# Kernel optimization log

Hardware: AMD Instinct MI355X
Metric: run time of the kernel (lower is better)

The kernel has to match this reference:

```python
import jax, jax.numpy as jnp
import numpy as np

ALPHA = 0.05        # per-layer ternary scale folded into the compact weight
FULL_OUT = 4096
FULL_IN = 4096
N_ROWS = 2048       # active (kept) output channels
N_COLS = 2048       # active (kept) input channels
B, S = 4, 2048


def setup_inputs() -> dict:
    key = jax.random.key(0)
    kx, kw, kb, kr, kc = jax.random.split(key, 5)
    x = jax.random.normal(kx, (B, S, FULL_IN), dtype=jnp.float32)
    compact_weight = jax.random.normal(kw, (N_ROWS, N_COLS), dtype=jnp.float32)
    bias = jax.random.normal(kb, (FULL_OUT,), dtype=jnp.float32)
    # unique, sorted index maps (compact -> full), as produced by from_linear
    active_rows = jnp.sort(jax.random.permutation(kr, FULL_OUT)[:N_ROWS]).astype(jnp.int64)
    active_cols = jnp.sort(jax.random.permutation(kc, FULL_IN)[:N_COLS]).astype(jnp.int64)
    return {
        "x": x,
        "compact_weight": compact_weight,
        "bias": bias,
        "active_rows": active_rows,
        "active_cols": active_cols,
    }


def reference(x, compact_weight, bias, active_rows, active_cols):
    # gather live input channels: [B, S, N_COLS]
    x_compact = jnp.take(x, active_cols, axis=-1)
    # compact GEMM with alpha-scaled ternary weight: [B, S, N_ROWS]
    w = compact_weight * ALPHA
    y_compact = jnp.einsum("bsc,rc->bsr", x_compact, w)
    # zero-scatter back to full output dim, then bias add
    y = jnp.zeros(x.shape[:-1] + (FULL_OUT,), dtype=y_compact.dtype)
    y = y.at[..., active_rows].set(y_compact)
    return y + bias
```

## Files before the change

kernel.cpp:

```cpp
#include <hip/hip_runtime.h>
#include <hip/hip_bf16.h>

#define ALPHA 0.05f

constexpr int FULL = 4096;
constexpr int Mtot = 8192;
constexpr int Kc   = 2048;
constexpr int Nc   = 2048;

typedef __hip_bfloat16 bf16_t;
using bf16x8 = __attribute__((ext_vector_type(8))) __bf16;
using f32x4  = __attribute__((ext_vector_type(4))) float;

__device__ __forceinline__ void gload_lds16(const bf16_t* g, bf16_t* l) {
  __builtin_amdgcn_global_load_lds(
      (const __attribute__((address_space(1))) void*)g,
      (__attribute__((address_space(3))) void*)l, 16, 0, 0);
}

__global__ __launch_bounds__(256)
void k_convert_x(const float* __restrict__ x, const int* __restrict__ cols,
                 bf16_t* __restrict__ A) {
  __shared__ float xr[FULL];
  const int m = blockIdx.x, t = threadIdx.x;
  const float4* xg = reinterpret_cast<const float4*>(x + (size_t)m * FULL);
  float4* xl = reinterpret_cast<float4*>(xr);
#pragma unroll
  for (int i = 0; i < FULL / 1024; ++i) xl[t + i * 256] = xg[t + i * 256];
  __syncthreads();
  const int4 c0 = reinterpret_cast<const int4*>(cols)[t * 2];
  const int4 c1 = reinterpret_cast<const int4*>(cols)[t * 2 + 1];
  bf16_t tmp[8];
  tmp[0] = __float2bfloat16(xr[c0.x]);
  tmp[1] = __float2bfloat16(xr[c0.y]);
  tmp[2] = __float2bfloat16(xr[c0.z]);
  tmp[3] = __float2bfloat16(xr[c0.w]);
  tmp[4] = __float2bfloat16(xr[c1.x]);
  tmp[5] = __float2bfloat16(xr[c1.y]);
  tmp[6] = __float2bfloat16(xr[c1.z]);
  tmp[7] = __float2bfloat16(xr[c1.w]);
  reinterpret_cast<uint4*>(A + (size_t)m * Kc)[t] =
      *reinterpret_cast<const uint4*>(tmp);
}

__global__ void k_convert_w(const float* __restrict__ w, bf16_t* __restrict__ Wb) {
  int idx = blockIdx.x * blockDim.x + threadIdx.x;
  const float4* src = reinterpret_cast<const float4*>(w) + (size_t)idx * 2;
  float4 v0 = src[0], v1 = src[1];
  bf16_t tmp[8];
  tmp[0] = __float2bfloat16(v0.x * ALPHA);
  tmp[1] = __float2bfloat16(v0.y * ALPHA);
  tmp[2] = __float2bfloat16(v0.z * ALPHA);
  tmp[3] = __float2bfloat16(v0.w * ALPHA);
  tmp[4] = __float2bfloat16(v1.x * ALPHA);
  tmp[5] = __float2bfloat16(v1.y * ALPHA);
  tmp[6] = __float2bfloat16(v1.z * ALPHA);
  tmp[7] = __float2bfloat16(v1.w * ALPHA);
  *reinterpret_cast<uint4*>(&Wb[(size_t)idx * 8]) =
      *reinterpret_cast<const uint4*>(tmp);
}

__global__ void k_bias_fill(const float* __restrict__ bias, float* __restrict__ out) {
  int idx = blockIdx.x * blockDim.x + threadIdx.x;
  const float4 v = reinterpret_cast<const float4*>(bias)[idx & (FULL / 4 - 1)];
  reinterpret_cast<float4*>(out)[idx] = v;
}

constexpr int BM2 = 256, BN2 = 128, BK2 = 64;
constexpr int NT2 = Kc / BK2;
constexpr int G_M2 = Mtot / BM2;
constexpr int G_N2 = Nc / BN2;
constexpr int NWG2 = G_M2 * G_N2;

__global__ __launch_bounds__(512, 1)
void k_gemm8(const bf16_t* __restrict__ A, const bf16_t* __restrict__ Wb,
             float* __restrict__ yc) {
  __shared__ __align__(16) bf16_t As[3][BM2 * BK2];
  __shared__ __align__(16) bf16_t Bs[3][BN2 * BK2];

  const int bid = blockIdx.x;
  const int xcd = bid & 7, lid = bid >> 3;
  const int st = lid >> 4, wi = lid & 15;
  const int gm0 = (xcd * 4 + (wi >> 2)) * BM2;
  const int gn0 = (st * 4 + (wi & 3)) * BN2;

  const int t = threadIdx.x;
  const int w = t >> 6, l = t & 63;
  const int wr = w >> 2, wc = w & 3;
  const int lr = l & 15, lq = l >> 4;
  const int swz = ((l & 7) ^ (l >> 3)) * 8;

  const bf16_t* aSrc = A  + (size_t)(gm0 + w * 8 + (l >> 3)) * Kc + swz;
  const bf16_t* bSrc = Wb + (size_t)(gn0 + w * 8 + (l >> 3)) * Kc + swz;

#define STAGE8(bi, k0)                                                        \
  do {                                                                        \
    _Pragma("unroll") for (int j = 0; j < 4; ++j)                             \
        gload_lds16(aSrc + (size_t)j * 64 * Kc + (k0),                        \
                    &As[bi][(j * 64 + w * 8) * 64]);                          \
    _Pragma("unroll") for (int j = 0; j < 2; ++j)                             \
        gload_lds16(bSrc + (size_t)j * 64 * Kc + (k0),                        \
                    &Bs[bi][(j * 64 + w * 8) * 64]);                          \
  } while (0)

  f32x4 acc[8][2] = {};

  STAGE8(0, 0);
  STAGE8(1, 64);
  asm volatile("s_waitcnt vmcnt(6)" ::: "memory");
  __builtin_amdgcn_s_barrier();
  __builtin_amdgcn_sched_barrier(0);

  for (int tt = 0; tt < NT2; ++tt) {
    const int cur = tt % 3;
    if (tt + 2 < NT2) {
      const int nb = (tt + 2) % 3;
      STAGE8(nb, (tt + 2) * BK2);
    }
    const bf16_t* Ab = As[cur];
    const bf16_t* Bb = Bs[cur];
#pragma unroll
    for (int kk = 0; kk < 2; ++kk) {
      const int ko = (kk * 32 + lq * 8) ^ ((l & 7) << 3);
      bf16x8 af[8], bf[2];
#pragma unroll
      for (int mi = 0; mi < 8; ++mi)
        af[mi] = *reinterpret_cast<const bf16x8*>(
            &Ab[(wr * 128 + mi * 16 + lr) * BK2 + ko]);
#pragma unroll
      for (int ni = 0; ni < 2; ++ni)
        bf[ni] = *reinterpret_cast<const bf16x8*>(
            &Bb[(wc * 32 + ni * 16 + lr) * BK2 + ko]);
      asm volatile("s_waitcnt lgkmcnt(0)" ::: "memory");
      __builtin_amdgcn_sched_barrier(0);
      __builtin_amdgcn_s_setprio(1);
#pragma unroll
      for (int mi = 0; mi < 8; ++mi)
#pragma unroll
        for (int ni = 0; ni < 2; ++ni)
          acc[mi][ni] = __builtin_amdgcn_mfma_f32_16x16x32_bf16(
              af[mi], bf[ni], acc[mi][ni], 0, 0, 0);
      __builtin_amdgcn_s_setprio(0);
      __builtin_amdgcn_sched_barrier(0);
    }
    if (tt + 2 < NT2)
      asm volatile("s_waitcnt vmcnt(6)" ::: "memory");
    else
      asm volatile("s_waitcnt vmcnt(0)" ::: "memory");
    __builtin_amdgcn_s_barrier();
    __builtin_amdgcn_sched_barrier(0);
  }
#undef STAGE8

  const int mbase = gm0 + wr * 128 + lq * 4;
  const int nbase = gn0 + wc * 32 + lr;
#pragma unroll
  for (int ni = 0; ni < 2; ++ni) {
    int n = nbase + ni * 16;
#pragma unroll
    for (int mi = 0; mi < 8; ++mi)
#pragma unroll
      for (int j = 0; j < 4; ++j)
        yc[(size_t)(mbase + mi * 16 + j) * Nc + n] = acc[mi][ni][j];
  }
}

constexpr int BM = 128, BN = 128, BK = 64;
constexpr int GRID_N = Nc / BN;
constexpr int NWG = GRID_N * (Mtot / BM);

__global__ __launch_bounds__(256)
void k_gemm_fb(const bf16_t* __restrict__ A, const bf16_t* __restrict__ Wb,
               const float* __restrict__ bias, const int* __restrict__ rows,
               float* __restrict__ out) {
  __shared__ __align__(16) bf16_t As[BM * BK];
  __shared__ __align__(16) bf16_t Bs[BN * BK];
  const int bid = blockIdx.x;
  const int wgid = (bid & 7) * (NWG / 8) + (bid >> 3);
  const int bm0 = (wgid / GRID_N) * BM, bn0 = (wgid % GRID_N) * BN;
  const int t = threadIdx.x;
  const int w = t >> 6, l = t & 63;
  const int wm = (w >> 1) * 64, wn = (w & 1) * 64;
  const bf16_t* srcA[4];
  const bf16_t* srcB[4];
#pragma unroll
  for (int i = 0; i < 4; ++i) {
    int elem = i * 2048 + t * 8;
    int row = elem >> 6, col = elem & 63;
    srcA[i] = A + (size_t)(bm0 + row) * Kc + col;
    srcB[i] = Wb + (size_t)(bn0 + row) * Kc + col;
  }
  f32x4 acc[4][4] = {};
  for (int k0 = 0; k0 < Kc; k0 += BK) {
#pragma unroll
    for (int i = 0; i < 4; ++i) {
      gload_lds16(srcA[i] + k0, As + i * 2048 + w * 512);
      gload_lds16(srcB[i] + k0, Bs + i * 2048 + w * 512);
    }
    __syncthreads();
    const int r = l & 15;
#pragma unroll
    for (int kk = 0; kk < 2; ++kk) {
      const int ko = kk * 32 + (l >> 4) * 8;
      bf16x8 af[4], bf[4];
#pragma unroll
      for (int mi = 0; mi < 4; ++mi)
        af[mi] = *reinterpret_cast<const bf16x8*>(&As[(wm + mi * 16 + r) * BK + ko]);
#pragma unroll
      for (int ni = 0; ni < 4; ++ni)
        bf[ni] = *reinterpret_cast<const bf16x8*>(&Bs[(wn + ni * 16 + r) * BK + ko]);
#pragma unroll
      for (int mi = 0; mi < 4; ++mi)
#pragma unroll
        for (int ni = 0; ni < 4; ++ni)
          acc[mi][ni] = __builtin_amdgcn_mfma_f32_16x16x32_bf16(
              af[mi], bf[ni], acc[mi][ni], 0, 0, 0);
    }
    __syncthreads();
  }
  const int lr = (l >> 4) * 4, lc = l & 15;
#pragma unroll
  for (int ni = 0; ni < 4; ++ni) {
    int nc = bn0 + wn + ni * 16 + lc;
    int oc = rows[nc];
    float bv = bias[oc];
#pragma unroll
    for (int mi = 0; mi < 4; ++mi)
#pragma unroll
      for (int j = 0; j < 4; ++j)
        out[(size_t)(bm0 + wm + mi * 16 + lr + j) * FULL + oc] =
            acc[mi][ni][j] + bv;
  }
}

__global__ __launch_bounds__(256)
void k_output(const float* __restrict__ yc, const float* __restrict__ bias,
              const int* __restrict__ rows, float* __restrict__ out) {
  __shared__ float row[FULL];
  const int m = blockIdx.x, t = threadIdx.x;
  const float4 z4 = {0.f, 0.f, 0.f, 0.f};
  float4* rl = reinterpret_cast<float4*>(row);
#pragma unroll
  for (int i = 0; i < FULL / 1024; ++i) rl[t + i * 256] = z4;
  __syncthreads();
  const float4* ycr = reinterpret_cast<const float4*>(yc + (size_t)m * Nc);
#pragma unroll
  for (int i = 0; i < Nc / 1024; ++i) {
    int idx = t + i * 256;
    float4 v = ycr[idx];
    int4 rr = reinterpret_cast<const int4*>(rows)[idx];
    row[rr.x] = v.x;
    row[rr.y] = v.y;
    row[rr.z] = v.z;
    row[rr.w] = v.w;
  }
  __syncthreads();
  float4* orow = reinterpret_cast<float4*>(out + (size_t)m * FULL);
  const float4* b4 = reinterpret_cast<const float4*>(bias);
#pragma unroll
  for (int i = 0; i < FULL / 1024; ++i) {
    int idx = t + i * 256;
    float4 r = rl[idx];
    float4 b = b4[idx];
    r.x += b.x; r.y += b.y; r.z += b.z; r.w += b.w;
    orow[idx] = r;
  }
}

__global__ void k_gemm_naive(const float* __restrict__ x, const float* __restrict__ wgt,
                             const float* __restrict__ bias, const int* __restrict__ rows,
                             const int* __restrict__ cols, float* __restrict__ out) {
  int idx = blockIdx.x * blockDim.x + threadIdx.x;
  int m = idx / Nc, n = idx - (idx / Nc) * Nc;
  const float* xr = x + (size_t)m * FULL;
  const float* wr = wgt + (size_t)n * Kc;
  float s = 0.f;
  for (int k = 0; k < Kc; ++k) s += xr[cols[k]] * wr[k];
  int oc = rows[n];
  out[(size_t)m * FULL + oc] = s * ALPHA + bias[oc];
}

extern "C" void kernel_launch(void* const* d_in, const int* in_sizes, int n_in,
                              void* d_out, int out_size, void* d_ws, size_t ws_size,
                              hipStream_t stream) {
  const float* x    = (const float*)d_in[0];
  const float* wgt  = (const float*)d_in[1];
  const float* bias = (const float*)d_in[2];
  const int*   rows = (const int*)d_in[3];
  const int*   cols = (const int*)d_in[4];
  float* out = (float*)d_out;

  const size_t needA = (size_t)Mtot * Kc * sizeof(bf16_t);
  const size_t needW = (size_t)Nc * Kc * sizeof(bf16_t);
  const size_t needY = (size_t)Mtot * Nc * sizeof(float);

  if (ws_size >= needA + needW + needY) {
    bf16_t* Abf = (bf16_t*)d_ws;
    bf16_t* Wbf = (bf16_t*)((char*)d_ws + needA);
    float*  yc  = (float*)((char*)d_ws + needA + needW);
    k_convert_x<<<Mtot, 256, 0, stream>>>(x, cols, Abf);
    k_convert_w<<<(Nc * (Kc / 8)) / 256, 256, 0, stream>>>(wgt, Wbf);
    k_gemm8<<<NWG2, 512, 0, stream>>>(Abf, Wbf, yc);
    k_output<<<Mtot, 256, 0, stream>>>(yc, bias, rows, out);
  } else if (ws_size >= needA + needW) {
    bf16_t* Abf = (bf16_t*)d_ws;
    bf16_t* Wbf = (bf16_t*)((char*)d_ws + needA);
    k_convert_x<<<Mtot, 256, 0, stream>>>(x, cols, Abf);
    k_convert_w<<<(Nc * (Kc / 8)) / 256, 256, 0, stream>>>(wgt, Wbf);
    k_bias_fill<<<(Mtot * (FULL / 4)) / 256, 256, 0, stream>>>(bias, out);
    k_gemm_fb<<<NWG, 256, 0, stream>>>(Abf, Wbf, bias, rows, out);
  } else {
    k_bias_fill<<<(Mtot * (FULL / 4)) / 256, 256, 0, stream>>>(bias, out);
    k_gemm_naive<<<(Mtot * Nc) / 256, 256, 0, stream>>>(x, wgt, bias, rows, cols, out);
  }
}
```

Before: 366.5 us.

## Enlarge GEMM tile to 256x256 with ping-pong schedule; batch rows in gather kernels

The main GEMM moves from 256x128 tiles with a triple buffer to 256x256 tiles with a double buffer. Each K step is split into four MFMA quadrants, with staged LDS reads and global-to-LDS prefetch interleaved through barriers. This raises arithmetic intensity per loaded byte and halves the workgroup count. The input-gather and output-scatter kernels now each process four rows per block, prefetching the next row into a second LDS buffer while the current one is handled. The risks are more accumulator registers, a complex barrier and waitcnt schedule that is easy to get wrong, and fewer workgroups to fill the CUs.

Result: faster. 343.9 us (-6.2%).

```diff
diff --git a/kernel.cpp b/kernel.cpp
--- a/kernel.cpp
+++ b/kernel.cpp
@@ -21,26 +21,45 @@
 __global__ __launch_bounds__(256)
 void k_convert_x(const float* __restrict__ x, const int* __restrict__ cols,
                  bf16_t* __restrict__ A) {
-  __shared__ float xr[FULL];
-  const int m = blockIdx.x, t = threadIdx.x;
-  const float4* xg = reinterpret_cast<const float4*>(x + (size_t)m * FULL);
-  float4* xl = reinterpret_cast<float4*>(xr);
-#pragma unroll
-  for (int i = 0; i < FULL / 1024; ++i) xl[t + i * 256] = xg[t + i * 256];
-  __syncthreads();
+  __shared__ float xr[2][FULL];
+  const int t = threadIdx.x;
+  const int m0 = blockIdx.x * 4;
   const int4 c0 = reinterpret_cast<const int4*>(cols)[t * 2];
   const int4 c1 = reinterpret_cast<const int4*>(cols)[t * 2 + 1];
-  bf16_t tmp[8];
-  tmp[0] = __float2bfloat16(xr[c0.x]);
-  tmp[1] = __float2bfloat16(xr[c0.y]);
-  tmp[2] = __float2bfloat16(xr[c0.z]);
-  tmp[3] = __float2bfloat16(xr[c0.w]);
-  tmp[4] = __float2bfloat16(xr[c1.x]);
-  tmp[5] = __float2bfloat16(xr[c1.y]);
-  tmp[6] = __float2bfloat16(xr[c1.z]);
-  tmp[7] = __float2bfloat16(xr[c1.w]);
-  reinterpret_cast<uint4*>(A + (size_t)m * Kc)[t] =
-      *reinterpret_cast<const uint4*>(tmp);
+  {
+    const float4* xg = reinterpret_cast<const float4*>(x + (size_t)m0 * FULL);
+    float4* xl = reinterpret_cast<float4*>(xr[0]);
+#pragma unroll
+    for (int i = 0; i < 4; ++i) xl[t + i * 256] = xg[t + i * 256];
+  }
+  __syncthreads();
+#pragma unroll
+  for (int r = 0; r < 4; ++r) {
+    float4 g0, g1, g2, g3;
+    if (r < 3) {
+      const float4* xn =
+          reinterpret_cast<const float4*>(x + (size_t)(m0 + r + 1) * FULL);
+      g0 = xn[t]; g1 = xn[t + 256]; g2 = xn[t + 512]; g3 = xn[t + 768];
+    }
+    const float* cur = xr[r & 1];
+    bf16_t tmp[8];
+    tmp[0] = __float2bfloat16(cur[c0.x]);
+    tmp[1] = __float2bfloat16(cur[c0.y]);
+    tmp[2] = __float2bfloat16(cur[c0.z]);
+    tmp[3] = __float2bfloat16(cur[c0.w]);
+    tmp[4] = __float2bfloat16(cur[c1.x]);
+    tmp[5] = __float2bfloat16(cur[c1.y]);
+    tmp[6] = __float2bfloat16(cur[c1.z]);
+    tmp[7] = __float2bfloat16(cur[c1.w]);
+    reinterpret_cast<uint4*>(A + (size_t)(m0 + r) * Kc)[t] =
+        *reinterpret_cast<const uint4*>(tmp);
+    if (r < 3) {
+      __syncthreads();
+      float4* xw = reinterpret_cast<float4*>(xr[(r + 1) & 1]);
+      xw[t] = g0; xw[t + 256] = g1; xw[t + 512] = g2; xw[t + 768] = g3;
+      __syncthreads();
+    }
+  }
 }
 
 __global__ void k_convert_w(const float* __restrict__ w, bf16_t* __restrict__ Wb) {
@@ -66,102 +85,225 @@
   reinterpret_cast<float4*>(out)[idx] = v;
 }
 
-constexpr int BM2 = 256, BN2 = 128, BK2 = 64;
-constexpr int NT2 = Kc / BK2;
-constexpr int G_M2 = Mtot / BM2;
-constexpr int G_N2 = Nc / BN2;
-constexpr int NWG2 = G_M2 * G_N2;
+constexpr int BM3 = 256, BN3 = 256, BK3 = 64;
+constexpr int NT3 = Kc / BK3;
+constexpr int NWG3 = (Mtot / BM3) * (Nc / BN3);
 
 __global__ __launch_bounds__(512, 1)
 void k_gemm8(const bf16_t* __restrict__ A, const bf16_t* __restrict__ Wb,
              float* __restrict__ yc) {
-  __shared__ __align__(16) bf16_t As[3][BM2 * BK2];
-  __shared__ __align__(16) bf16_t Bs[3][BN2 * BK2];
+  __shared__ __align__(16) bf16_t As3[2][BM3 * BK3];
+  __shared__ __align__(16) bf16_t Bs3[2][BN3 * BK3];
 
   const int bid = blockIdx.x;
   const int xcd = bid & 7, lid = bid >> 3;
-  const int st = lid >> 4, wi = lid & 15;
-  const int gm0 = (xcd * 4 + (wi >> 2)) * BM2;
-  const int gn0 = (st * 4 + (wi & 3)) * BN2;
+  const int gm0 = (xcd * 4 + (lid >> 3)) * BM3;
+  const int gn0 = (lid & 7) * BN3;
 
   const int t = threadIdx.x;
   const int w = t >> 6, l = t & 63;
+  const int w8 = w * 8;
   const int wr = w >> 2, wc = w & 3;
   const int lr = l & 15, lq = l >> 4;
+  const int xorv = (l & 7) << 3;
   const int swz = ((l & 7) ^ (l >> 3)) * 8;
 
-  const bf16_t* aSrc = A  + (size_t)(gm0 + w * 8 + (l >> 3)) * Kc + swz;
-  const bf16_t* bSrc = Wb + (size_t)(gn0 + w * 8 + (l >> 3)) * Kc + swz;
-
-#define STAGE8(bi, k0)                                                        \
-  do {                                                                        \
-    _Pragma("unroll") for (int j = 0; j < 4; ++j)                             \
-        gload_lds16(aSrc + (size_t)j * 64 * Kc + (k0),                        \
-                    &As[bi][(j * 64 + w * 8) * 64]);                          \
-    _Pragma("unroll") for (int j = 0; j < 2; ++j)                             \
-        gload_lds16(bSrc + (size_t)j * 64 * Kc + (k0),                        \
-                    &Bs[bi][(j * 64 + w * 8) * 64]);                          \
+  const bf16_t* aB = A  + (size_t)(gm0 + w8 + (l >> 3)) * Kc + swz;
+  const bf16_t* bB = Wb + (size_t)(gn0 + w8 + (l >> 3)) * Kc + swz;
+
+#define STG_A(bi, half, kt)                                                     \
+  do {                                                                          \
+    gload_lds16(aB + (size_t)((half) * 128) * Kc + (kt) * 64,                   \
+                &As3[bi][(((half) * 128) + w8) * 64]);                          \
+    gload_lds16(aB + (size_t)((half) * 128 + 64) * Kc + (kt) * 64,              \
+                &As3[bi][(((half) * 128 + 64) + w8) * 64]);                     \
   } while (0)
-
-  f32x4 acc[8][2] = {};
-
-  STAGE8(0, 0);
-  STAGE8(1, 64);
+#define STG_B(bi, half, kt)                                                     \
+  do {                                                                          \
+    gload_lds16(bB + (size_t)((half) * 128) * Kc + (kt) * 64,                   \
+                &Bs3[bi][(((half) * 128) + w8) * 64]);                          \
+    gload_lds16(bB + (size_t)((half) * 128 + 64) * Kc + (kt) * 64,              \
+                &Bs3[bi][(((half) * 128 + 64) + w8) * 64]);                     \
+  } while (0)
+
+  f32x4 acc[8][4] = {};
+  bf16x8 afl[4][2], afh[4][2], bfl[2][2], bfh[2][2];
+
+  STG_A(0, 0, 0); STG_A(0, 1, 0); STG_B(0, 0, 0); STG_B(0, 1, 0);
+  STG_B(1, 0, 1); STG_A(1, 0, 1); STG_A(1, 1, 1);
   asm volatile("s_waitcnt vmcnt(6)" ::: "memory");
   __builtin_amdgcn_s_barrier();
   __builtin_amdgcn_sched_barrier(0);
 
-  for (int tt = 0; tt < NT2; ++tt) {
-    const int cur = tt % 3;
-    if (tt + 2 < NT2) {
-      const int nb = (tt + 2) % 3;
-      STAGE8(nb, (tt + 2) * BK2);
-    }
-    const bf16_t* Ab = As[cur];
-    const bf16_t* Bb = Bs[cur];
-#pragma unroll
-    for (int kk = 0; kk < 2; ++kk) {
-      const int ko = (kk * 32 + lq * 8) ^ ((l & 7) << 3);
-      bf16x8 af[8], bf[2];
-#pragma unroll
-      for (int mi = 0; mi < 8; ++mi)
-        af[mi] = *reinterpret_cast<const bf16x8*>(
-            &Ab[(wr * 128 + mi * 16 + lr) * BK2 + ko]);
+  for (int tt = 0; tt < NT3; ++tt) {
+    const int cur = tt & 1, nxt = cur ^ 1;
+    const bf16_t* Ap = As3[cur];
+    const bf16_t* Bp = Bs3[cur];
+
+#pragma unroll
+    for (int mi = 0; mi < 4; ++mi)
+#pragma unroll
+      for (int kk = 0; kk < 2; ++kk)
+        afl[mi][kk] = *reinterpret_cast<const bf16x8*>(
+            &Ap[(wr * 128 + mi * 16 + lr) * 64 + ((kk * 32 + lq * 8) ^ xorv)]);
+#pragma unroll
+    for (int ni = 0; ni < 2; ++ni)
+#pragma unroll
+      for (int kk = 0; kk < 2; ++kk)
+        bfl[ni][kk] = *reinterpret_cast<const bf16x8*>(
+            &Bp[(wc * 64 + ni * 16 + lr) * 64 + ((kk * 32 + lq * 8) ^ xorv)]);
+    if (tt + 1 < NT3) STG_B(nxt, 1, tt + 1);
+    asm volatile("s_waitcnt lgkmcnt(8)" ::: "memory");
+    __builtin_amdgcn_s_barrier();
+    asm volatile("s_waitcnt lgkmcnt(0)" ::: "memory");
+    __builtin_amdgcn_sched_barrier(0);
+    __builtin_amdgcn_s_setprio(1);
+#pragma unroll
+    for (int mi = 0; mi < 4; ++mi)
 #pragma unroll
       for (int ni = 0; ni < 2; ++ni)
-        bf[ni] = *reinterpret_cast<const bf16x8*>(
-            &Bb[(wc * 32 + ni * 16 + lr) * BK2 + ko]);
-      asm volatile("s_waitcnt lgkmcnt(0)" ::: "memory");
-      __builtin_amdgcn_sched_barrier(0);
-      __builtin_amdgcn_s_setprio(1);
-#pragma unroll
-      for (int mi = 0; mi < 8; ++mi)
-#pragma unroll
-        for (int ni = 0; ni < 2; ++ni)
+#pragma unroll
+        for (int kk = 0; kk < 2; ++kk)
           acc[mi][ni] = __builtin_amdgcn_mfma_f32_16x16x32_bf16(
-              af[mi], bf[ni], acc[mi][ni], 0, 0, 0);
-      __builtin_amdgcn_s_setprio(0);
-      __builtin_amdgcn_sched_barrier(0);
-    }
-    if (tt + 2 < NT2)
+              afl[mi][kk], bfl[ni][kk], acc[mi][ni], 0, 0, 0);
+    __builtin_amdgcn_s_setprio(0);
+    __builtin_amdgcn_s_barrier();
+
+#pragma unroll
+    for (int ni = 0; ni < 2; ++ni)
+#pragma unroll
+      for (int kk = 0; kk < 2; ++kk)
+        bfh[ni][kk] = *reinterpret_cast<const bf16x8*>(
+            &Bp[(wc * 64 + (ni + 2) * 16 + lr) * 64 +
+                ((kk * 32 + lq * 8) ^ xorv)]);
+    __builtin_amdgcn_s_barrier();
+    asm volatile("s_waitcnt lgkmcnt(0)" ::: "memory");
+    __builtin_amdgcn_sched_barrier(0);
+    __builtin_amdgcn_s_setprio(1);
+#pragma unroll
+    for (int mi = 0; mi < 4; ++mi)
+#pragma unroll
+      for (int ni = 0; ni < 2; ++ni)
+#pragma unroll
+        for (int kk = 0; kk < 2; ++kk)
+          acc[mi][ni + 2] = __builtin_amdgcn_mfma_f32_16x16x32_bf16(
+              afl[mi][kk], bfh[ni][kk], acc[mi][ni + 2], 0, 0, 0);
+    __builtin_amdgcn_s_setprio(0);
+    __builtin_amdgcn_s_barrier();
+
+#pragma unroll
+    for (int mi = 0; mi < 4; ++mi)
+#pragma unroll
+      for (int kk = 0; kk < 2; ++kk)
+        afh[mi][kk] = *reinterpret_cast<const bf16x8*>(
+            &Ap[(wr * 128 + (mi + 4) * 16 + lr) * 64 +
+                ((kk * 32 + lq * 8) ^ xorv)]);
+    if (tt + 2 < NT3) STG_B(cur, 0, tt + 2);
+    __builtin_amdgcn_s_barrier();
+    asm volatile("s_waitcnt lgkmcnt(0)" ::: "memory");
+    __builtin_amdgcn_sched_barrier(0);
+    __builtin_amdgcn_s_setprio(1);
+#pragma unroll
+    for (int mi = 0; mi < 4; ++mi)
+#pragma unroll
+      for (int ni = 0; ni < 2; ++ni)
+#pragma unroll
+        for (int kk = 0; kk < 2; ++kk)
+          acc[mi + 4][ni + 2] = __builtin_amdgcn_mfma_f32_16x16x32_bf16(
+              afh[mi][kk], bfh[ni][kk], acc[mi + 4][ni + 2], 0, 0, 0);
+    __builtin_amdgcn_s_setprio(0);
+    __builtin_amdgcn_s_barrier();
+
+    if (tt + 2 < NT3) { STG_A(cur, 0, tt + 2); STG_A(cur, 1, tt + 2); }
+    __builtin_amdgcn_s_barrier();
+    __builtin_amdgcn_s_setprio(1);
+#pragma unroll
+    for (int mi = 0; mi < 4; ++mi)
+#pragma unroll
+      for (int ni = 0; ni < 2; ++ni)
+#pragma unroll
+        for (int kk = 0; kk < 2; ++kk)
+          acc[mi + 4][ni] = __builtin_amdgcn_mfma_f32_16x16x32_bf16(
+              afh[mi][kk], bfl[ni][kk], acc[mi + 4][ni], 0, 0, 0);
+    __builtin_amdgcn_s_setprio(0);
+    if (tt + 2 < NT3)
       asm volatile("s_waitcnt vmcnt(6)" ::: "memory");
-    else
+    else if (tt + 1 < NT3)
       asm volatile("s_waitcnt vmcnt(0)" ::: "memory");
     __builtin_amdgcn_s_barrier();
     __builtin_amdgcn_sched_barrier(0);
   }
-#undef STAGE8
+#undef STG_A
+#undef STG_B
 
   const int mbase = gm0 + wr * 128 + lq * 4;
-  const int nbase = gn0 + wc * 32 + lr;
-#pragma unroll
-  for (int ni = 0; ni < 2; ++ni) {
+  const int nbase = gn0 + wc * 64 + lr;
+#pragma unroll
+  for (int ni = 0; ni < 4; ++ni) {
     int n = nbase + ni * 16;
 #pragma unroll
     for (int mi = 0; mi < 8; ++mi)
 #pragma unroll
       for (int j = 0; j < 4; ++j)
         yc[(size_t)(mbase + mi * 16 + j) * Nc + n] = acc[mi][ni][j];
+  }
+}
+
+__global__ __launch_bounds__(256)
+void k_output(const float* __restrict__ yc, const float* __restrict__ bias,
+              const int* __restrict__ rows, float* __restrict__ out) {
+  __shared__ float rbuf[2][FULL];
+  const int t = threadIdx.x;
+  const int m0 = blockIdx.x * 4;
+  const int4 ra = reinterpret_cast<const int4*>(rows)[t];
+  const int4 rb = reinterpret_cast<const int4*>(rows)[t + 256];
+  float4 bv0 = reinterpret_cast<const float4*>(bias)[t];
+  float4 bv1 = reinterpret_cast<const float4*>(bias)[t + 256];
+  float4 bv2 = reinterpret_cast<const float4*>(bias)[t + 512];
+  float4 bv3 = reinterpret_cast<const float4*>(bias)[t + 768];
+
+  {
+    const float4 z4 = {0.f, 0.f, 0.f, 0.f};
+    float4* rl = reinterpret_cast<float4*>(rbuf[0]);
+#pragma unroll
+    for (int i = 0; i < 4; ++i) rl[t + i * 256] = z4;
+    __syncthreads();
+    const float4* ycr = reinterpret_cast<const float4*>(yc + (size_t)m0 * Nc);
+    float4 ya = ycr[t], yb = ycr[t + 256];
+    rbuf[0][ra.x] = ya.x; rbuf[0][ra.y] = ya.y;
+    rbuf[0][ra.z] = ya.z; rbuf[0][ra.w] = ya.w;
+    rbuf[0][rb.x] = yb.x; rbuf[0][rb.y] = yb.y;
+    rbuf[0][rb.z] = yb.z; rbuf[0][rb.w] = yb.w;
+    __syncthreads();
+  }
+#pragma unroll
+  for (int r = 0; r < 4; ++r) {
+    const int cur = r & 1, nx = cur ^ 1;
+    float4 ya, yb;
+    if (r < 3) {
+      const float4* ycn =
+          reinterpret_cast<const float4*>(yc + (size_t)(m0 + r + 1) * Nc);
+      ya = ycn[t]; yb = ycn[t + 256];
+      const float4 z4 = {0.f, 0.f, 0.f, 0.f};
+      float4* rl = reinterpret_cast<float4*>(rbuf[nx]);
+#pragma unroll
+      for (int i = 0; i < 4; ++i) rl[t + i * 256] = z4;
+    }
+    __syncthreads();
+    float4* orow = reinterpret_cast<float4*>(out + (size_t)(m0 + r) * FULL);
+    const float4* rl = reinterpret_cast<const float4*>(rbuf[cur]);
+    float4 v0 = rl[t], v1 = rl[t + 256], v2 = rl[t + 512], v3 = rl[t + 768];
+    v0.x += bv0.x; v0.y += bv0.y; v0.z += bv0.z; v0.w += bv0.w;
+    v1.x += bv1.x; v1.y += bv1.y; v1.z += bv1.z; v1.w += bv1.w;
+    v2.x += bv2.x; v2.y += bv2.y; v2.z += bv2.z; v2.w += bv2.w;
+    v3.x += bv3.x; v3.y += bv3.y; v3.z += bv3.z; v3.w += bv3.w;
+    orow[t] = v0; orow[t + 256] = v1; orow[t + 512] = v2; orow[t + 768] = v3;
+    if (r < 3) {
+      float* rn = rbuf[nx];
+      rn[ra.x] = ya.x; rn[ra.y] = ya.y; rn[ra.z] = ya.z; rn[ra.w] = ya.w;
+      rn[rb.x] = yb.x; rn[rb.y] = yb.y; rn[rb.z] = yb.z; rn[rb.w] = yb.w;
+      __syncthreads();
+    }
   }
 }
 
@@ -233,40 +375,6 @@
   }
 }
 
-__global__ __launch_bounds__(256)
-void k_output(const float* __restrict__ yc, const float* __restrict__ bias,
-              const int* __restrict__ rows, float* __restrict__ out) {
-  __shared__ float row[FULL];
-  const int m = blockIdx.x, t = threadIdx.x;
-  const float4 z4 = {0.f, 0.f, 0.f, 0.f};
-  float4* rl = reinterpret_cast<float4*>(row);
-#pragma unroll
-  for (int i = 0; i < FULL / 1024; ++i) rl[t + i * 256] = z4;
-  __syncthreads();
-  const float4* ycr = reinterpret_cast<const float4*>(yc + (size_t)m * Nc);
-#pragma unroll
-  for (int i = 0; i < Nc / 1024; ++i) {
-    int idx = t + i * 256;
-    float4 v = ycr[idx];
-    int4 rr = reinterpret_cast<const int4*>(rows)[idx];
-    row[rr.x] = v.x;
-    row[rr.y] = v.y;
-    row[rr.z] = v.z;
-    row[rr.w] = v.w;
-  }
-  __syncthreads();
-  float4* orow = reinterpret_cast<float4*>(out + (size_t)m * FULL);
-  const float4* b4 = reinterpret_cast<const float4*>(bias);
-#pragma unroll
-  for (int i = 0; i < FULL / 1024; ++i) {
-    int idx = t + i * 256;
-    float4 r = rl[idx];
-    float4 b = b4[idx];
-    r.x += b.x; r.y += b.y; r.z += b.z; r.w += b.w;
-    orow[idx] = r;
-  }
-}
-
 __global__ void k_gemm_naive(const float* __restrict__ x, const float* __restrict__ wgt,
                              const float* __restrict__ bias, const int* __restrict__ rows,
                              const int* __restrict__ cols, float* __restrict__ out) {
@@ -298,14 +406,14 @@
     bf16_t* Abf = (bf16_t*)d_ws;
     bf16_t* Wbf = (bf16_t*)((char*)d_ws + needA);
     float*  yc  = (float*)((char*)d_ws + needA + needW);
-    k_convert_x<<<Mtot, 256, 0, stream>>>(x, cols, Abf);
+    k_convert_x<<<Mtot / 4, 256, 0, stream>>>(x, cols, Abf);
     k_convert_w<<<(Nc * (Kc / 8)) / 256, 256, 0, stream>>>(wgt, Wbf);
-    k_gemm8<<<NWG2, 512, 0, stream>>>(Abf, Wbf, yc);
-    k_output<<<Mtot, 256, 0, stream>>>(yc, bias, rows, out);
+    k_gemm8<<<NWG3, 512, 0, stream>>>(Abf, Wbf, yc);
+    k_output<<<Mtot / 4, 256, 0, stream>>>(yc, bias, rows, out);
   } else if (ws_size >= needA + needW) {
     bf16_t* Abf = (bf16_t*)d_ws;
     bf16_t* Wbf = (bf16_t*)((char*)d_ws + needA);
-    k_convert_x<<<Mtot, 256, 0, stream>>>(x, cols, Abf);
+    k_convert_x<<<Mtot / 4, 256, 0, stream>>>(x, cols, Abf);
     k_convert_w<<<(Nc * (Kc / 8)) / 256, 256, 0, stream>>>(wgt, Wbf);
     k_bias_fill<<<(Mtot * (FULL / 4)) / 256, 256, 0, stream>>>(bias, out);
     k_gemm_fb<<<NWG, 256, 0, stream>>>(Abf, Wbf, bias, rows, out);
```
